# Kernel optimization log

Measured on AMD Instinct MI355X. Metric: run time of the kernel, lower is better.

## Reference

```python
import jax, jax.numpy as jnp
import numpy as np

B, T, D, O = 4, 1024, 256, 256


def setup_inputs() -> dict:
    key = jax.random.key(0)
    kx, kw = jax.random.split(key)
    x = jax.random.normal(kx, (B, T, D), dtype=jnp.float32)
    # he_normal init: stddev = sqrt(2 / fan_in), stacked per-position kernels [T, D, O]
    W = jax.random.normal(kw, (T, D, O), dtype=jnp.float32) * np.sqrt(2.0 / D).astype(np.float32)
    return {"x": x, "W": W}


def reference(x, W):
    # Original loop: out[:, i, :] = mean_{t<=i} (x[:, t, :] @ W[i])
    # = (cumulative mean of x along T) @ per-position kernel W[i].
    t = x.shape[1]
    counts = jnp.arange(1, t + 1, dtype=x.dtype)[:, None]  # (T,1)
    cm = jnp.cumsum(x, axis=1) / counts                    # (B,T,D) cumulative mean
    return jnp.einsum('btd,tdo->bto', cm, W)               # (B,T,O)
```

## Files before the change

### kernel.cpp

```cpp
#include <hip/hip_runtime.h>

#define B_ 4
#define T_ 1024
#define D_ 256
#define O_ 256
#define NC 32
#define CL 32

typedef float v4f __attribute__((ext_vector_type(4)));

__global__ __launch_bounds__(256) void chunk_sums(const float* __restrict__ x,
                                                  float* __restrict__ S) {
    const int d  = threadIdx.x;
    const int bc = blockIdx.x;
    const int b  = bc / NC;
    const int c  = bc % NC;
    const float* xp = x + ((size_t)b * T_ + (size_t)c * CL) * D_ + d;
    float s = 0.f;
#pragma unroll
    for (int i = 0; i < CL; ++i) s += xp[(size_t)i * D_];
    S[((size_t)b * NC + c) * D_ + d] = s;
}

__global__ __launch_bounds__(256) void cumsum_mean(const float* __restrict__ x,
                                                   const float* __restrict__ S,
                                                   float* __restrict__ cm) {
    const int d  = threadIdx.x;
    const int bc = blockIdx.x;
    const int b  = bc / NC;
    const int c  = bc % NC;
    float off = 0.f;
#pragma unroll
    for (int cc = 0; cc < NC; ++cc) {
        const float v = S[((size_t)b * NC + cc) * D_ + d];
        off += (cc < c) ? v : 0.f;
    }
    const float* xp = x  + ((size_t)b * T_ + (size_t)c * CL) * D_ + d;
    float*       cp = cm + ((size_t)b * T_ + (size_t)c * CL) * D_ + d;
    float run = off;
#pragma unroll 4
    for (int i = 0; i < CL; ++i) {
        run += xp[(size_t)i * D_];
        const int t = c * CL + i;
        cp[(size_t)i * D_] = run / (float)(t + 1);
    }
}

__global__ __launch_bounds__(256) void gemm_t(const float* __restrict__ cm,
                                              const float* __restrict__ W,
                                              float* __restrict__ out) {
    const int t0  = blockIdx.x * 4;
    const int tid = threadIdx.x;
    const int tq  = tid >> 6;
    const int oq  = tid & 63;

    __shared__ float cml[4][D_][4];

#pragma unroll
    for (int q = 0; q < 4; ++q)
#pragma unroll
        for (int b = 0; b < 4; ++b)
            cml[q][tid][b] = cm[((size_t)b * T_ + t0 + q) * D_ + tid];
    __syncthreads();

    const v4f* Wp = (const v4f*)(W + (size_t)(t0 + tq) * D_ * O_) + oq;

    v4f a0 = (v4f)(0.f), a1 = (v4f)(0.f), a2 = (v4f)(0.f), a3 = (v4f)(0.f);

    v4f w[16];
#pragma unroll
    for (int j = 0; j < 8; ++j)
        w[j] = __builtin_nontemporal_load(Wp + (size_t)j * (O_ / 4));

#pragma unroll 1
    for (int dd = 0; dd < D_; dd += 16) {
#pragma unroll
        for (int j = 0; j < 8; ++j)
            w[8 + j] = __builtin_nontemporal_load(Wp + (size_t)(dd + 8 + j) * (O_ / 4));
#pragma unroll
        for (int j = 0; j < 8; ++j) {
            const v4f c4 = *(const v4f*)cml[tq][dd + j];
            a0 += c4.x * w[j]; a1 += c4.y * w[j]; a2 += c4.z * w[j]; a3 += c4.w * w[j];
        }
        if (dd + 16 < D_) {
#pragma unroll
            for (int j = 0; j < 8; ++j)
                w[j] = __builtin_nontemporal_load(Wp + (size_t)(dd + 16 + j) * (O_ / 4));
        }
#pragma unroll
        for (int j = 0; j < 8; ++j) {
            const v4f c4 = *(const v4f*)cml[tq][dd + 8 + j];
            a0 += c4.x * w[8 + j]; a1 += c4.y * w[8 + j];
            a2 += c4.z * w[8 + j]; a3 += c4.w * w[8 + j];
        }
    }

    const size_t obase = (size_t)(t0 + tq) * O_ + (size_t)oq * 4;
    __builtin_nontemporal_store(a0, (v4f*)&out[(size_t)0 * T_ * O_ + obase]);
    __builtin_nontemporal_store(a1, (v4f*)&out[(size_t)1 * T_ * O_ + obase]);
    __builtin_nontemporal_store(a2, (v4f*)&out[(size_t)2 * T_ * O_ + obase]);
    __builtin_nontemporal_store(a3, (v4f*)&out[(size_t)3 * T_ * O_ + obase]);
}

extern "C" void kernel_launch(void* const* d_in, const int* in_sizes, int n_in,
                              void* d_out, int out_size, void* d_ws, size_t ws_size,
                              hipStream_t stream) {
    const float* x = (const float*)d_in[0];
    const float* W = (const float*)d_in[1];
    float* out = (float*)d_out;

    float* cm = (float*)d_ws;
    float* S  = (float*)d_ws + (size_t)B_ * T_ * D_;

    chunk_sums <<<B_ * NC, 256, 0, stream>>>(x, S);
    cumsum_mean<<<B_ * NC, 256, 0, stream>>>(x, S, cm);
    gemm_t     <<<T_ / 4,  256, 0, stream>>>(cm, W, out);
}
```

Before: 343.9 us.

## Split GEMM reduction dimension across waves and deepen W load pipeline

Each block now handles 2 time positions instead of 4, and the D reduction for each position is split between two waves. The halves are combined through shared memory before the store. The grid doubles to 512 blocks so more CUs stream W concurrently. The register prefetch becomes a 4-stage ring that keeps 3 batches of 8 loads in flight, fully unrolled. The cost is an extra LDS reduction and a second barrier, with half the threads idle at the store.

```diff
diff --git a/kernel.cpp b/kernel.cpp
--- a/kernel.cpp
+++ b/kernel.cpp
@@ -46,60 +46,75 @@
     }
 }
 
-__global__ __launch_bounds__(256) void gemm_t(const float* __restrict__ cm,
-                                              const float* __restrict__ W,
-                                              float* __restrict__ out) {
-    const int t0  = blockIdx.x * 4;
+__global__ __launch_bounds__(256, 2) void gemm_t(const float* __restrict__ cm,
+                                                 const float* __restrict__ W,
+                                                 float* __restrict__ out) {
+    const int t0  = blockIdx.x * 2;
     const int tid = threadIdx.x;
-    const int tq  = tid >> 6;
+    const int wv  = tid >> 6;
+    const int tq  = wv >> 1;
+    const int h   = wv & 1;
     const int oq  = tid & 63;
 
-    __shared__ float cml[4][D_][4];
+    __shared__ float cml[2][D_][4];
+    __shared__ float red[2][16][64];
 
 #pragma unroll
-    for (int q = 0; q < 4; ++q)
+    for (int q = 0; q < 2; ++q)
 #pragma unroll
         for (int b = 0; b < 4; ++b)
             cml[q][tid][b] = cm[((size_t)b * T_ + t0 + q) * D_ + tid];
     __syncthreads();
 
-    const v4f* Wp = (const v4f*)(W + (size_t)(t0 + tq) * D_ * O_) + oq;
+    const v4f* Wp = (const v4f*)(W + ((size_t)(t0 + tq) * D_ + (size_t)h * 128) * O_) + oq;
 
     v4f a0 = (v4f)(0.f), a1 = (v4f)(0.f), a2 = (v4f)(0.f), a3 = (v4f)(0.f);
 
-    v4f w[16];
+    v4f w[4][8];
 #pragma unroll
-    for (int j = 0; j < 8; ++j)
-        w[j] = __builtin_nontemporal_load(Wp + (size_t)j * (O_ / 4));
-
-#pragma unroll 1
-    for (int dd = 0; dd < D_; dd += 16) {
+    for (int st = 0; st < 3; ++st)
 #pragma unroll
         for (int j = 0; j < 8; ++j)
-            w[8 + j] = __builtin_nontemporal_load(Wp + (size_t)(dd + 8 + j) * (O_ / 4));
+            w[st][j] = __builtin_nontemporal_load(Wp + (size_t)(st * 8 + j) * (O_ / 4));
+
+#pragma unroll
+    for (int s = 0; s < 16; ++s) {
+        const int ld = s + 3;
+        if (ld < 16) {
+#pragma unroll
+            for (int j = 0; j < 8; ++j)
+                w[ld & 3][j] =
+                    __builtin_nontemporal_load(Wp + (size_t)(ld * 8 + j) * (O_ / 4));
+        }
+        const int db = h * 128 + s * 8;
 #pragma unroll
         for (int j = 0; j < 8; ++j) {
-            const v4f c4 = *(const v4f*)cml[tq][dd + j];
-            a0 += c4.x * w[j]; a1 += c4.y * w[j]; a2 += c4.z * w[j]; a3 += c4.w * w[j];
-        }
-        if (dd + 16 < D_) {
-#pragma unroll
-            for (int j = 0; j < 8; ++j)
-                w[j] = __builtin_nontemporal_load(Wp + (size_t)(dd + 16 + j) * (O_ / 4));
-        }
-#pragma unroll
-        for (int j = 0; j < 8; ++j) {
-            const v4f c4 = *(const v4f*)cml[tq][dd + 8 + j];
-            a0 += c4.x * w[8 + j]; a1 += c4.y * w[8 + j];
-            a2 += c4.z * w[8 + j]; a3 += c4.w * w[8 + j];
+            const v4f c4 = *(const v4f*)cml[tq][db + j];
+            a0 += c4.x * w[s & 3][j];
+            a1 += c4.y * w[s & 3][j];
+            a2 += c4.z * w[s & 3][j];
+            a3 += c4.w * w[s & 3][j];
         }
     }
 
-    const size_t obase = (size_t)(t0 + tq) * O_ + (size_t)oq * 4;
-    __builtin_nontemporal_store(a0, (v4f*)&out[(size_t)0 * T_ * O_ + obase]);
-    __builtin_nontemporal_store(a1, (v4f*)&out[(size_t)1 * T_ * O_ + obase]);
-    __builtin_nontemporal_store(a2, (v4f*)&out[(size_t)2 * T_ * O_ + obase]);
-    __builtin_nontemporal_store(a3, (v4f*)&out[(size_t)3 * T_ * O_ + obase]);
+    if (h == 1) {
+        red[tq][ 0][oq] = a0.x; red[tq][ 1][oq] = a0.y; red[tq][ 2][oq] = a0.z; red[tq][ 3][oq] = a0.w;
+        red[tq][ 4][oq] = a1.x; red[tq][ 5][oq] = a1.y; red[tq][ 6][oq] = a1.z; red[tq][ 7][oq] = a1.w;
+        red[tq][ 8][oq] = a2.x; red[tq][ 9][oq] = a2.y; red[tq][10][oq] = a2.z; red[tq][11][oq] = a2.w;
+        red[tq][12][oq] = a3.x; red[tq][13][oq] = a3.y; red[tq][14][oq] = a3.z; red[tq][15][oq] = a3.w;
+    }
+    __syncthreads();
+    if (h == 0) {
+        a0.x += red[tq][ 0][oq]; a0.y += red[tq][ 1][oq]; a0.z += red[tq][ 2][oq]; a0.w += red[tq][ 3][oq];
+        a1.x += red[tq][ 4][oq]; a1.y += red[tq][ 5][oq]; a1.z += red[tq][ 6][oq]; a1.w += red[tq][ 7][oq];
+        a2.x += red[tq][ 8][oq]; a2.y += red[tq][ 9][oq]; a2.z += red[tq][10][oq]; a2.w += red[tq][11][oq];
+        a3.x += red[tq][12][oq]; a3.y += red[tq][13][oq]; a3.z += red[tq][14][oq]; a3.w += red[tq][15][oq];
+        const size_t obase = (size_t)(t0 + tq) * O_ + (size_t)oq * 4;
+        __builtin_nontemporal_store(a0, (v4f*)&out[(size_t)0 * T_ * O_ + obase]);
+        __builtin_nontemporal_store(a1, (v4f*)&out[(size_t)1 * T_ * O_ + obase]);
+        __builtin_nontemporal_store(a2, (v4f*)&out[(size_t)2 * T_ * O_ + obase]);
+        __builtin_nontemporal_store(a3, (v4f*)&out[(size_t)3 * T_ * O_ + obase]);
+    }
 }
 
 extern "C" void kernel_launch(void* const* d_in, const int* in_sizes, int n_in,
@@ -114,5 +129,5 @@
 
     chunk_sums <<<B_ * NC, 256, 0, stream>>>(x, S);
     cumsum_mean<<<B_ * NC, 256, 0, stream>>>(x, S, cm);
-    gemm_t     <<<T_ / 4,  256, 0, stream>>>(cm, W, out);
+    gemm_t     <<<T_ / 2,  256, 0, stream>>>(cm, W, out);
 }
```

Result: no change. 346.3 us (+0.7%).
